# Performance work log

Hardware: AMD Instinct MI355X
Metric: run time of the kernel (lower is better)

Reference implementation:

```python
import jax, jax.numpy as jnp
import numpy as np

DIM = 1024
NUM_HEADS = 16
HEAD_DIM = DIM // NUM_HEADS
B, S = 2, 2048


def setup_inputs() -> dict:
    key = jax.random.key(0)
    ks = jax.random.split(key, 7)
    x = jax.random.normal(ks[0], (B, S, DIM), dtype=jnp.float32)
    cos = jax.random.uniform(ks[1], (S, HEAD_DIM // 2), dtype=jnp.float32)
    sin = jax.random.uniform(ks[2], (S, HEAD_DIM // 2), dtype=jnp.float32)
    scale = 1.0 / np.sqrt(DIM)
    Wq = jax.random.normal(ks[3], (DIM, DIM), dtype=jnp.float32) * scale
    Wk = jax.random.normal(ks[4], (DIM, DIM), dtype=jnp.float32) * scale
    Wv = jax.random.normal(ks[5], (DIM, DIM), dtype=jnp.float32) * scale
    Wo = jax.random.normal(ks[6], (DIM, DIM), dtype=jnp.float32) * scale
    return {"x": x, "cos": cos, "sin": sin, "Wq": Wq, "Wk": Wk, "Wv": Wv, "Wo": Wo}


def _apply_rope(t, c, s):
    # t: [B, S, H, hd]; c, s: [1, S, 1, hd] (already doubled)
    half = t.shape[-1] // 2
    t1, t2 = t[..., :half], t[..., half:]
    rot = jnp.concatenate([-t2, t1], axis=-1)
    return t * c + rot * s


def reference(x, cos, sin, Wq, Wk, Wv, Wo):
    Bs, Ss, D = x.shape
    H, hd = NUM_HEADS, HEAD_DIM
    q = (x @ Wq).reshape(Bs, Ss, H, hd)
    k = (x @ Wk).reshape(Bs, Ss, H, hd)
    v = (x @ Wv).reshape(Bs, Ss, H, hd)
    # repeat(1,1,1,2) in torch tiles cos as [cos, cos] along last dim
    c = jnp.concatenate([cos, cos], axis=-1)[None, :, None, :]
    s = jnp.concatenate([sin, sin], axis=-1)[None, :, None, :]
    q = _apply_rope(q, c, s)
    k = _apply_rope(k, c, s)
    # SDPA, non-causal, scale 1/sqrt(hd)
    scores = jnp.einsum("bqhd,bkhd->bhqk", q, k) / jnp.sqrt(jnp.float32(hd))
    attn = jax.nn.softmax(scores, axis=-1)
    out = jnp.einsum("bhqk,bkhd->bqhd", attn, v).reshape(Bs, Ss, D)
    return out @ Wo
```

## Files before the change

### kernel.cpp

```cpp
#include <hip/hip_runtime.h>

#define B_  2
#define S_  2048
#define D_  1024
#define H_  16
#define HD_ 64
#define M_  (B_*S_)

typedef __bf16 bf16x8 __attribute__((ext_vector_type(8)));
typedef float  f32x4  __attribute__((ext_vector_type(4)));
typedef float  f32x16 __attribute__((ext_vector_type(16)));
typedef unsigned short ushort_t;

static __device__ __forceinline__ ushort_t f2bf(float f) {
  __bf16 b = (__bf16)f;
  return __builtin_bit_cast(ushort_t, b);
}
static __device__ __forceinline__ float bf2f(ushort_t u) {
  return (float)__builtin_bit_cast(__bf16, u);
}

typedef __attribute__((address_space(1))) const unsigned u32g;
typedef __attribute__((address_space(3))) unsigned u32l;
static __device__ __forceinline__ void gll16(const ushort_t* g, __bf16* l) {
  __builtin_amdgcn_global_load_lds((u32g*)g, (u32l*)l, 16, 0, 0);
}

__global__ __launch_bounds__(256) void convert_x(const float* __restrict__ x,
                                                 ushort_t* __restrict__ xb) {
  size_t e = ((size_t)blockIdx.x * 256 + threadIdx.x) * 8;
  float4 a = *(const float4*)(x + e);
  float4 b = *(const float4*)(x + e + 4);
  uint4 pk;
  pk.x = (unsigned)f2bf(a.x) | ((unsigned)f2bf(a.y) << 16);
  pk.y = (unsigned)f2bf(a.z) | ((unsigned)f2bf(a.w) << 16);
  pk.z = (unsigned)f2bf(b.x) | ((unsigned)f2bf(b.y) << 16);
  pk.w = (unsigned)f2bf(b.z) | ((unsigned)f2bf(b.w) << 16);
  *(uint4*)(xb + e) = pk;
}

__global__ __launch_bounds__(256) void transpose_w(const float* __restrict__ Wq,
                                                   const float* __restrict__ Wk,
                                                   const float* __restrict__ Wv,
                                                   const float* __restrict__ Wo,
                                                   ushort_t* __restrict__ Wqkvt,
                                                   ushort_t* __restrict__ Wot) {
  __shared__ __bf16 T[64][72];
  const int z = blockIdx.z;
  const float* W = (z == 0) ? Wq : (z == 1) ? Wk : (z == 2) ? Wv : Wo;
  ushort_t* Wt = (z < 3) ? (Wqkvt + (size_t)z * 1048576) : Wot;
  const int k0 = blockIdx.y * 64, n0 = blockIdx.x * 64;
  const int t = threadIdx.x, r = t >> 2, c16 = (t & 3) * 16;
#pragma unroll
  for (int i = 0; i < 4; i++) {
    float4 v = *(const float4*)(W + (size_t)(k0 + r) * D_ + n0 + c16 + i * 4);
    T[r][c16 + i*4 + 0] = (__bf16)v.x;
    T[r][c16 + i*4 + 1] = (__bf16)v.y;
    T[r][c16 + i*4 + 2] = (__bf16)v.z;
    T[r][c16 + i*4 + 3] = (__bf16)v.w;
  }
  __syncthreads();
  ushort_t vals[16];
#pragma unroll
  for (int i = 0; i < 16; i++) vals[i] = __builtin_bit_cast(ushort_t, T[c16 + i][r]);
  ushort_t* dst = Wt + (size_t)(n0 + r) * D_ + k0 + c16;
  *(uint4*)dst       = *(const uint4*)&vals[0];
  *(uint4*)(dst + 8) = *(const uint4*)&vals[8];
}

__global__ __launch_bounds__(256) void transpose_v(const ushort_t* __restrict__ Vb,
                                                   ushort_t* __restrict__ Vtg) {
  __shared__ __bf16 T[64][72];
  const int bh = blockIdx.y, kt = blockIdx.x;
  const int t = threadIdx.x, r = t >> 2, c16 = (t & 3) * 16;
  const ushort_t* src = Vb + ((size_t)bh * S_ + kt*64 + r) * 64 + c16;
  *(uint4*)&T[r][c16]     = *(const uint4*)src;
  *(uint4*)&T[r][c16 + 8] = *(const uint4*)(src + 8);
  __syncthreads();
  ushort_t vals[16];
#pragma unroll
  for (int i = 0; i < 16; i++) {
    int c = c16 + i;
    int k = ((c & 1) << 5) | (c >> 1);
    vals[i] = __builtin_bit_cast(ushort_t, T[k][r]);
  }
  ushort_t* dst = Vtg + ((size_t)bh * 64 + r) * S_ + kt*64 + c16;
  *(uint4*)dst       = *(const uint4*)&vals[0];
  *(uint4*)(dst + 8) = *(const uint4*)&vals[8];
}

template<int OMODE, int BN>
__global__ __launch_bounds__(256) void gemm_bf16(const ushort_t* __restrict__ A,
                                                 const ushort_t* __restrict__ Bt,
                                                 void* __restrict__ Cp,
                                                 const float* __restrict__ cosb,
                                                 const float* __restrict__ sinb) {
  constexpr int NF = BN / 32;
  __shared__ __bf16 As[4096];
  __shared__ __bf16 Bs[BN * 32];
  const int t = threadIdx.x, w = t >> 6, lane = t & 63, l15 = lane & 15, g = lane >> 4;
  const int wr = w >> 1, wc = w & 1;
  const int row0 = blockIdx.y * 128, col0 = blockIdx.x * BN;
  const int lr = t >> 2, lc = (t & 3) * 8;
  f32x4 acc[4][NF] = {};

  for (int k0 = 0; k0 < D_; k0 += 32) {
    __syncthreads();
#pragma unroll
    for (int i = 0; i < 2; i++)
      gll16(A + (size_t)(row0 + i*64 + lr) * D_ + k0 + lc, &As[i*2048 + w*512]);
#pragma unroll
    for (int i = 0; i < BN/64; i++)
      gll16(Bt + (size_t)(col0 + i*64 + lr) * D_ + k0 + lc, &Bs[i*2048 + w*512]);
    __syncthreads();
    bf16x8 af[4], bfv[NF];
#pragma unroll
    for (int mt = 0; mt < 4; mt++)  af[mt]  = *(const bf16x8*)&As[(wr*64 + mt*16 + l15)*32 + g*8];
#pragma unroll
    for (int nt = 0; nt < NF; nt++) bfv[nt] = *(const bf16x8*)&Bs[(wc*(BN/2) + nt*16 + l15)*32 + g*8];
#pragma unroll
    for (int mt = 0; mt < 4; mt++)
#pragma unroll
      for (int nt = 0; nt < NF; nt++)
        acc[mt][nt] = __builtin_amdgcn_mfma_f32_16x16x32_bf16(af[mt], bfv[nt], acc[mt][nt], 0, 0, 0);
  }

  if (OMODE == 0) {
#pragma unroll
    for (int mt = 0; mt < 4; mt++)
#pragma unroll
      for (int nt = 0; nt < NF; nt++) {
        int col = col0 + wc*(BN/2) + nt*16 + l15;
#pragma unroll
        for (int reg = 0; reg < 4; reg++) {
          int r = row0 + wr*64 + mt*16 + g*4 + reg;
          ((float*)Cp)[(size_t)r * D_ + col] = acc[mt][nt][reg];
        }
      }
  } else {
    const int mat = col0 >> 10;
    const int nc0 = (col0 + wc*64) & 1023;
    const int h = nc0 >> 6;
    ushort_t* dst = (ushort_t*)Cp + (size_t)mat * 4194304;
    const float QS = 0.125f * 1.4426950408889634f;
#pragma unroll
    for (int mt = 0; mt < 4; mt++) {
#pragma unroll
      for (int reg = 0; reg < 4; reg++) {
        int r = row0 + wr*64 + mt*16 + g*4 + reg;
        int b = r >> 11, s = r & (S_ - 1);
        size_t base = (((size_t)(b*H_ + h) * S_ + s) << 6);
        if (mat < 2) {
#pragma unroll
          for (int nt = 0; nt < 2; nt++) {
            int d1 = nt*16 + l15;
            float c  = cosb[s*32 + d1];
            float sn = sinb[s*32 + d1];
            float v1 = acc[mt][nt][reg], v2 = acc[mt][nt+2][reg];
            float r1 = v1*c - v2*sn;
            float r2 = v2*c + v1*sn;
            if (mat == 0) { r1 *= QS; r2 *= QS; }
            dst[base + d1]      = f2bf(r1);
            dst[base + d1 + 32] = f2bf(r2);
          }
        } else {
#pragma unroll
          for (int nt = 0; nt < 4; nt++)
            dst[base + nt*16 + l15] = f2bf(acc[mt][nt][reg]);
        }
      }
    }
  }
}

__global__ __launch_bounds__(256) void attn32(const ushort_t* __restrict__ Q,
                                              const ushort_t* __restrict__ K,
                                              const ushort_t* __restrict__ Vtg,
                                              ushort_t* __restrict__ op0,
                                              ushort_t* __restrict__ op1,
                                              float* __restrict__ lw) {
  __shared__ __bf16 KsL[128 * 64];
  __shared__ __bf16 VtL[64 * 128];
  __shared__ __bf16 Ps[4][32][72];
  const int t = threadIdx.x, w = t >> 6, lane = t & 63;
  const int l31 = lane & 31, h2 = lane >> 5, sw = l31 & 7;
  const int bh = blockIdx.y, q0 = blockIdx.x * 128 + w * 32, z = blockIdx.z;

  const ushort_t* Qp = Q + ((size_t)bh * S_ + q0 + l31) * HD_;
  bf16x8 qf[4];
#pragma unroll
  for (int kc = 0; kc < 4; kc++) qf[kc] = *(const bf16x8*)(Qp + kc*16 + h2*8);

  f32x16 o0 = {}, o1 = {};
  float lp[16];
#pragma unroll
  for (int i = 0; i < 16; i++) lp[i] = 0.f;

  const ushort_t* Kb = K   + ((size_t)bh * S_ + z * 1024) * HD_;
  const ushort_t* Vg = Vtg + (size_t)bh * HD_ * S_ + z * 1024;

  const int krl = lane >> 3;
  const int kco = ((lane & 7) ^ krl) * 8;
  const int vrl = lane >> 4;

  for (int kt = 0; kt < 8; kt++) {
    __syncthreads();
#pragma unroll
    for (int p = 0; p < 4; p++) {
      int bk = w*8 + p*32;
      gll16(Kb + (size_t)(kt*128 + bk + krl) * HD_ + kco, &KsL[(bk)*64]);
    }
#pragma unroll
    for (int p = 0; p < 4; p++) {
      int bd = w*4 + p*16;
      int d  = bd + vrl;
      int cd = (lane & 8) | ((lane & 7) ^ (d & 7));
      gll16(Vg + (size_t)d * S_ + kt*128 + cd*8, &VtL[(bd)*128]);
    }
    __syncthreads();

#pragma unroll
    for (int ph = 0; ph < 2; ph++) {
      f32x16 s0 = {}, s1 = {};
#pragma unroll
      for (int kc = 0; kc < 4; kc++) {
        int c = kc*2 + h2;
        int cs = (c ^ sw) * 8;
        bf16x8 b0 = *(const bf16x8*)&KsL[(ph*64 + l31)*64      + cs];
        bf16x8 b1 = *(const bf16x8*)&KsL[(ph*64 + 32 + l31)*64 + cs];
        s0 = __builtin_amdgcn_mfma_f32_32x32x16_bf16(qf[kc], b0, s0, 0, 0, 0);
        s1 = __builtin_amdgcn_mfma_f32_32x32x16_bf16(qf[kc], b1, s1, 0, 0, 0);
      }

#pragma unroll
      for (int i = 0; i < 16; i++) {
        float p0 = __builtin_amdgcn_exp2f(s0[i]);
        float p1 = __builtin_amdgcn_exp2f(s1[i]);
        lp[i] += p0 + p1;
        int row = (i & 3) + 8*(i >> 2) + 4*h2;
        unsigned pk = (unsigned)f2bf(p0) | ((unsigned)f2bf(p1) << 16);
        *(unsigned*)&Ps[w][row][2*l31] = pk;
      }

#pragma unroll
      for (int kc = 0; kc < 4; kc++) {
        int c = kc*2 + h2;
        int cs = (ph*8 | (c ^ sw)) * 8;
        bf16x8 pf = *(const bf16x8*)&Ps[w][l31][kc*16 + h2*8];
        bf16x8 v0 = *(const bf16x8*)&VtL[(l31)*128      + cs];
        bf16x8 v1 = *(const bf16x8*)&VtL[(32 + l31)*128 + cs];
        o0 = __builtin_amdgcn_mfma_f32_32x32x16_bf16(pf, v0, o0, 0, 0, 0);
        o1 = __builtin_amdgcn_mfma_f32_32x32x16_bf16(pf, v1, o1, 0, 0, 0);
      }
    }
  }

#pragma unroll
  for (int i = 0; i < 16; i++) {
#pragma unroll
    for (int mk = 1; mk < 32; mk <<= 1) lp[i] += __shfl_xor(lp[i], mk, 64);
  }

  ushort_t* op = (z == 0) ? op0 : op1;
  float* lwp = lw + (size_t)(z*32 + bh) * S_;
#pragma unroll
  for (int i = 0; i < 16; i++) {
    int row = q0 + (i & 3) + 8*(i >> 2) + 4*h2;
    size_t base = ((size_t)bh * S_ + row) * 64;
    op[base + l31]      = f2bf(o0[i]);
    op[base + 32 + l31] = f2bf(o1[i]);
    if (l31 == 0) lwp[row] = lp[i];
  }
}

__global__ __launch_bounds__(256) void combine(const ushort_t* __restrict__ op0,
                                               const ushort_t* __restrict__ op1,
                                               const float* __restrict__ lw,
                                               ushort_t* __restrict__ att) {
  int tid = blockIdx.x * 256 + threadIdx.x;
  int d8 = (tid & 7) * 8;
  int s  = (tid >> 3) & (S_ - 1);
  int bh = tid >> 14;
  size_t pb = ((size_t)bh * S_ + s) * 64 + d8;
  uint4 a = *(const uint4*)(op0 + pb);
  uint4 b = *(const uint4*)(op1 + pb);
  float inv = 1.f / (lw[(size_t)bh * S_ + s] + lw[(size_t)(32 + bh) * S_ + s]);
  const ushort_t* as = (const ushort_t*)&a;
  const ushort_t* bs = (const ushort_t*)&b;
  ushort_t outv[8];
#pragma unroll
  for (int i = 0; i < 8; i++)
    outv[i] = f2bf((bf2f(as[i]) + bf2f(bs[i])) * inv);
  int bidx = bh >> 4, h = bh & 15;
  *(uint4*)(att + ((size_t)(bidx * S_ + s)) * D_ + h*64 + d8) = *(const uint4*)outv;
}

extern "C" void kernel_launch(void* const* d_in, const int* in_sizes, int n_in,
                              void* d_out, int out_size, void* d_ws, size_t ws_size,
                              hipStream_t stream) {
  (void)in_sizes; (void)n_in; (void)out_size; (void)ws_size;
  const float* x    = (const float*)d_in[0];
  const float* cosb = (const float*)d_in[1];
  const float* sinb = (const float*)d_in[2];
  const float* Wq   = (const float*)d_in[3];
  const float* Wk   = (const float*)d_in[4];
  const float* Wv   = (const float*)d_in[5];
  const float* Wo   = (const float*)d_in[6];
  float* out = (float*)d_out;

  ushort_t* w     = (ushort_t*)d_ws;
  ushort_t* xb    = w;
  ushort_t* Wqkvt = w + 4194304;
  ushort_t* Wot   = w + 7340032;
  ushort_t* Qb    = w + 8388608;
  ushort_t* Kb    = w + 12582912;
  ushort_t* Vb    = w + 16777216;
  ushort_t* Vtg   = w + 20971520;
  ushort_t* att   = w + 25165824;
  float*    lw    = (float*)Wqkvt;

  convert_x<<<2048, 256, 0, stream>>>(x, xb);
  transpose_w<<<dim3(16, 16, 4), 256, 0, stream>>>(Wq, Wk, Wv, Wo, Wqkvt, Wot);

  gemm_bf16<1,128><<<dim3(24, 32), 256, 0, stream>>>(xb, Wqkvt, Qb, cosb, sinb);

  transpose_v<<<dim3(32, 32), 256, 0, stream>>>(Vb, Vtg);

  attn32<<<dim3(16, 32, 2), 256, 0, stream>>>(Qb, Kb, Vtg, xb, Vb, lw);

  combine<<<2048, 256, 0, stream>>>(xb, Vb, lw, att);

  gemm_bf16<0,64><<<dim3(16, 32), 256, 0, stream>>>(att, Wot, out, nullptr, nullptr);
}
```

Baseline: 214.5 us.

## Swap GEMM operand roles with LDS-staged coalesced epilogue and double-buffer attention K/V

```diff
diff --git a/kernel.cpp b/kernel.cpp
--- a/kernel.cpp
+++ b/kernel.cpp
@@ -89,39 +89,41 @@
   *(uint4*)(dst + 8) = *(const uint4*)&vals[8];
 }
 
-template<int OMODE, int BN>
-__global__ __launch_bounds__(256) void gemm_bf16(const ushort_t* __restrict__ A,
-                                                 const ushort_t* __restrict__ Bt,
+template<int OMODE, int BS>
+__global__ __launch_bounds__(256) void gemm_bf16(const ushort_t* __restrict__ Wt,
+                                                 const ushort_t* __restrict__ X,
                                                  void* __restrict__ Cp,
                                                  const float* __restrict__ cosb,
                                                  const float* __restrict__ sinb) {
-  constexpr int NF = BN / 32;
-  __shared__ __bf16 As[4096];
-  __shared__ __bf16 Bs[BN * 32];
+  constexpr int NT = BS / 32;
+  constexpr int SM = (OMODE == 1) ? 16384 : 6144;
+  __shared__ __bf16 SMEM[SM];
+  __bf16* As = SMEM;
+  __bf16* Bs = SMEM + 4096;
   const int t = threadIdx.x, w = t >> 6, lane = t & 63, l15 = lane & 15, g = lane >> 4;
   const int wr = w >> 1, wc = w & 1;
-  const int row0 = blockIdx.y * 128, col0 = blockIdx.x * BN;
-  const int lr = t >> 2, lc = (t & 3) * 8;
-  f32x4 acc[4][NF] = {};
+  const int f0 = blockIdx.y * 128, s0 = blockIdx.x * BS;
+  const int al = lane >> 2, ac = (lane & 3) * 8;
+  f32x4 acc[4][NT] = {};
 
   for (int k0 = 0; k0 < D_; k0 += 32) {
     __syncthreads();
 #pragma unroll
     for (int i = 0; i < 2; i++)
-      gll16(A + (size_t)(row0 + i*64 + lr) * D_ + k0 + lc, &As[i*2048 + w*512]);
-#pragma unroll
-    for (int i = 0; i < BN/64; i++)
-      gll16(Bt + (size_t)(col0 + i*64 + lr) * D_ + k0 + lc, &Bs[i*2048 + w*512]);
+      gll16(Wt + (size_t)(f0 + i*64 + w*16 + al) * D_ + k0 + ac, &As[i*2048 + w*512]);
+#pragma unroll
+    for (int i = 0; i < BS/64; i++)
+      gll16(X + (size_t)(s0 + i*64 + w*16 + al) * D_ + k0 + ac, &Bs[i*2048 + w*512]);
     __syncthreads();
-    bf16x8 af[4], bfv[NF];
+    bf16x8 af[4], bfv[NT];
 #pragma unroll
     for (int mt = 0; mt < 4; mt++)  af[mt]  = *(const bf16x8*)&As[(wr*64 + mt*16 + l15)*32 + g*8];
 #pragma unroll
-    for (int nt = 0; nt < NF; nt++) bfv[nt] = *(const bf16x8*)&Bs[(wc*(BN/2) + nt*16 + l15)*32 + g*8];
+    for (int nt = 0; nt < NT; nt++) bfv[nt] = *(const bf16x8*)&Bs[(wc*(BS/2) + nt*16 + l15)*32 + g*8];
 #pragma unroll
     for (int mt = 0; mt < 4; mt++)
 #pragma unroll
-      for (int nt = 0; nt < NF; nt++)
+      for (int nt = 0; nt < NT; nt++)
         acc[mt][nt] = __builtin_amdgcn_mfma_f32_16x16x32_bf16(af[mt], bfv[nt], acc[mt][nt], 0, 0, 0);
   }
 
@@ -129,46 +131,61 @@
 #pragma unroll
     for (int mt = 0; mt < 4; mt++)
 #pragma unroll
-      for (int nt = 0; nt < NF; nt++) {
-        int col = col0 + wc*(BN/2) + nt*16 + l15;
-#pragma unroll
-        for (int reg = 0; reg < 4; reg++) {
-          int r = row0 + wr*64 + mt*16 + g*4 + reg;
-          ((float*)Cp)[(size_t)r * D_ + col] = acc[mt][nt][reg];
-        }
+      for (int nt = 0; nt < NT; nt++) {
+        int s = s0 + wc*(BS/2) + nt*16 + l15;
+        int f = f0 + wr*64 + mt*16 + g*4;
+        *(float4*)&((float*)Cp)[(size_t)s * D_ + f] = *(float4*)&acc[mt][nt];
       }
   } else {
-    const int mat = col0 >> 10;
-    const int nc0 = (col0 + wc*64) & 1023;
-    const int h = nc0 >> 6;
+    const int hid = blockIdx.y*2 + wr;
+    const int mat = hid >> 4, h = hid & 15;
+    const int s0w = s0 + wc*64;
     ushort_t* dst = (ushort_t*)Cp + (size_t)mat * 4194304;
     const float QS = 0.125f * 1.4426950408889634f;
-#pragma unroll
-    for (int mt = 0; mt < 4; mt++) {
-#pragma unroll
-      for (int reg = 0; reg < 4; reg++) {
-        int r = row0 + wr*64 + mt*16 + g*4 + reg;
-        int b = r >> 11, s = r & (S_ - 1);
-        size_t base = (((size_t)(b*H_ + h) * S_ + s) << 6);
-        if (mat < 2) {
-#pragma unroll
-          for (int nt = 0; nt < 2; nt++) {
-            int d1 = nt*16 + l15;
-            float c  = cosb[s*32 + d1];
-            float sn = sinb[s*32 + d1];
-            float v1 = acc[mt][nt][reg], v2 = acc[mt][nt+2][reg];
-            float r1 = v1*c - v2*sn;
-            float r2 = v2*c + v1*sn;
+    if (mat < 2) {
+#pragma unroll
+      for (int mt = 0; mt < 2; mt++)
+#pragma unroll
+        for (int nt = 0; nt < 4; nt++) {
+          int s  = s0w + nt*16 + l15;
+          int sq = s & (S_ - 1);
+          float4 c4 = *(const float4*)&cosb[sq*32 + mt*16 + g*4];
+          float4 s4 = *(const float4*)&sinb[sq*32 + mt*16 + g*4];
+          const float* cf = (const float*)&c4;
+          const float* sf = (const float*)&s4;
+#pragma unroll
+          for (int r = 0; r < 4; r++) {
+            float v1 = acc[mt][nt][r], v2 = acc[mt+2][nt][r];
+            float r1 = v1*cf[r] - v2*sf[r];
+            float r2 = v2*cf[r] + v1*sf[r];
             if (mat == 0) { r1 *= QS; r2 *= QS; }
-            dst[base + d1]      = f2bf(r1);
-            dst[base + d1 + 32] = f2bf(r2);
+            acc[mt][nt][r] = r1; acc[mt+2][nt][r] = r2;
           }
-        } else {
-#pragma unroll
-          for (int nt = 0; nt < 4; nt++)
-            dst[base + nt*16 + l15] = f2bf(acc[mt][nt][reg]);
         }
+    }
+    __syncthreads();
+    __bf16* Tw = SMEM + w*4096;
+#pragma unroll
+    for (int mt = 0; mt < 4; mt++)
+#pragma unroll
+      for (int nt = 0; nt < 4; nt++) {
+        int s_loc = nt*16 + l15;
+        int d0 = mt*16 + g*4;
+        int ch = (d0 >> 3) ^ (s_loc & 7);
+        ushort_t pk[4];
+#pragma unroll
+        for (int r = 0; r < 4; r++) pk[r] = f2bf(acc[mt][nt][r]);
+        *(ushort4*)&Tw[s_loc*64 + ch*8 + (d0 & 7)] = *(const ushort4*)pk;
       }
+#pragma unroll
+    for (int j = 0; j < 8; j++) {
+      int s_loc = j*8 + (lane >> 3);
+      int ci = lane & 7;
+      int ch = ci ^ (s_loc & 7);
+      uint4 v = *(const uint4*)&Tw[s_loc*64 + ch*8];
+      int s = s0w + s_loc;
+      int b = s >> 11, srow = s & (S_ - 1);
+      *(uint4*)&dst[(((size_t)(b*H_ + h) * S_ + srow) << 6) + ci*8] = v;
     }
   }
 }
@@ -179,8 +196,8 @@
                                               ushort_t* __restrict__ op0,
                                               ushort_t* __restrict__ op1,
                                               float* __restrict__ lw) {
-  __shared__ __bf16 KsL[128 * 64];
-  __shared__ __bf16 VtL[64 * 128];
+  __shared__ __bf16 KsL[2][64 * 64];
+  __shared__ __bf16 VtL[2][64 * 64];
   __shared__ __bf16 Ps[4][32][72];
   const int t = threadIdx.x, w = t >> 6, lane = t & 63;
   const int l31 = lane & 31, h2 = lane >> 5, sw = l31 & 7;
@@ -198,62 +215,69 @@
 
   const ushort_t* Kb = K   + ((size_t)bh * S_ + z * 1024) * HD_;
   const ushort_t* Vg = Vtg + (size_t)bh * HD_ * S_ + z * 1024;
-
   const int krl = lane >> 3;
   const int kco = ((lane & 7) ^ krl) * 8;
-  const int vrl = lane >> 4;
-
-  for (int kt = 0; kt < 8; kt++) {
-    __syncthreads();
-#pragma unroll
-    for (int p = 0; p < 4; p++) {
-      int bk = w*8 + p*32;
-      gll16(Kb + (size_t)(kt*128 + bk + krl) * HD_ + kco, &KsL[(bk)*64]);
-    }
-#pragma unroll
-    for (int p = 0; p < 4; p++) {
-      int bd = w*4 + p*16;
-      int d  = bd + vrl;
-      int cd = (lane & 8) | ((lane & 7) ^ (d & 7));
-      gll16(Vg + (size_t)d * S_ + kt*128 + cd*8, &VtL[(bd)*128]);
-    }
-    __syncthreads();
-
-#pragma unroll
-    for (int ph = 0; ph < 2; ph++) {
-      f32x16 s0 = {}, s1 = {};
-#pragma unroll
-      for (int kc = 0; kc < 4; kc++) {
-        int c = kc*2 + h2;
-        int cs = (c ^ sw) * 8;
-        bf16x8 b0 = *(const bf16x8*)&KsL[(ph*64 + l31)*64      + cs];
-        bf16x8 b1 = *(const bf16x8*)&KsL[(ph*64 + 32 + l31)*64 + cs];
-        s0 = __builtin_amdgcn_mfma_f32_32x32x16_bf16(qf[kc], b0, s0, 0, 0, 0);
-        s1 = __builtin_amdgcn_mfma_f32_32x32x16_bf16(qf[kc], b1, s1, 0, 0, 0);
-      }
-
-#pragma unroll
-      for (int i = 0; i < 16; i++) {
-        float p0 = __builtin_amdgcn_exp2f(s0[i]);
-        float p1 = __builtin_amdgcn_exp2f(s1[i]);
-        lp[i] += p0 + p1;
-        int row = (i & 3) + 8*(i >> 2) + 4*h2;
-        unsigned pk = (unsigned)f2bf(p0) | ((unsigned)f2bf(p1) << 16);
-        *(unsigned*)&Ps[w][row][2*l31] = pk;
-      }
-
-#pragma unroll
-      for (int kc = 0; kc < 4; kc++) {
-        int c = kc*2 + h2;
-        int cs = (ph*8 | (c ^ sw)) * 8;
-        bf16x8 pf = *(const bf16x8*)&Ps[w][l31][kc*16 + h2*8];
-        bf16x8 v0 = *(const bf16x8*)&VtL[(l31)*128      + cs];
-        bf16x8 v1 = *(const bf16x8*)&VtL[(32 + l31)*128 + cs];
-        o0 = __builtin_amdgcn_mfma_f32_32x32x16_bf16(pf, v0, o0, 0, 0, 0);
-        o1 = __builtin_amdgcn_mfma_f32_32x32x16_bf16(pf, v1, o1, 0, 0, 0);
-      }
-    }
-  }
+
+  asm volatile("s_waitcnt vmcnt(0)" ::: "memory");
+
+#define STAGE(KT, CB)                                                        \
+  {                                                                          \
+    _Pragma("unroll")                                                        \
+    for (int p = 0; p < 2; p++) {                                            \
+      int bk = w*8 + p*32;                                                   \
+      gll16(Kb + (size_t)((KT)*64 + bk + krl) * HD_ + kco, &KsL[CB][bk*64]); \
+    }                                                                        \
+    _Pragma("unroll")                                                        \
+    for (int p = 0; p < 2; p++) {                                            \
+      int bd = w*8 + p*32;                                                   \
+      gll16(Vg + (size_t)(bd + krl) * S_ + (KT)*64 + kco, &VtL[CB][bd*64]);  \
+    }                                                                        \
+  }
+
+  STAGE(0, 0);
+  for (int kt = 0; kt < 16; kt++) {
+    const int cur = kt & 1;
+    if (kt < 15) {
+      STAGE(kt + 1, cur ^ 1);
+      asm volatile("s_waitcnt vmcnt(4)" ::: "memory");
+    } else {
+      asm volatile("s_waitcnt vmcnt(0)" ::: "memory");
+    }
+    asm volatile("s_barrier" ::: "memory");
+
+    f32x16 s0 = {}, s1 = {};
+#pragma unroll
+    for (int kc = 0; kc < 4; kc++) {
+      int cs = ((kc*2 + h2) ^ sw) * 8;
+      bf16x8 b0 = *(const bf16x8*)&KsL[cur][l31*64 + cs];
+      bf16x8 b1 = *(const bf16x8*)&KsL[cur][(32 + l31)*64 + cs];
+      s0 = __builtin_amdgcn_mfma_f32_32x32x16_bf16(qf[kc], b0, s0, 0, 0, 0);
+      s1 = __builtin_amdgcn_mfma_f32_32x32x16_bf16(qf[kc], b1, s1, 0, 0, 0);
+    }
+
+#pragma unroll
+    for (int i = 0; i < 16; i++) {
+      float p0 = __builtin_amdgcn_exp2f(s0[i]);
+      float p1 = __builtin_amdgcn_exp2f(s1[i]);
+      lp[i] += p0 + p1;
+      int row = (i & 3) + 8*(i >> 2) + 4*h2;
+      unsigned pk = (unsigned)f2bf(p0) | ((unsigned)f2bf(p1) << 16);
+      *(unsigned*)&Ps[w][row][2*l31] = pk;
+    }
+
+#pragma unroll
+    for (int kc = 0; kc < 4; kc++) {
+      int cs = ((kc*2 + h2) ^ sw) * 8;
+      bf16x8 pf = *(const bf16x8*)&Ps[w][l31][kc*16 + h2*8];
+      bf16x8 v0 = *(const bf16x8*)&VtL[cur][l31*64 + cs];
+      bf16x8 v1 = *(const bf16x8*)&VtL[cur][(32 + l31)*64 + cs];
+      o0 = __builtin_amdgcn_mfma_f32_32x32x16_bf16(pf, v0, o0, 0, 0, 0);
+      o1 = __builtin_amdgcn_mfma_f32_32x32x16_bf16(pf, v1, o1, 0, 0, 0);
+    }
+
+    asm volatile("s_barrier" ::: "memory");
+  }
+#undef STAGE
 
 #pragma unroll
   for (int i = 0; i < 16; i++) {
@@ -322,7 +346,7 @@
   convert_x<<<2048, 256, 0, stream>>>(x, xb);
   transpose_w<<<dim3(16, 16, 4), 256, 0, stream>>>(Wq, Wk, Wv, Wo, Wqkvt, Wot);
 
-  gemm_bf16<1,128><<<dim3(24, 32), 256, 0, stream>>>(xb, Wqkvt, Qb, cosb, sinb);
+  gemm_bf16<1,128><<<dim3(32, 24), 256, 0, stream>>>(Wqkvt, xb, Qb, cosb, sinb);
 
   transpose_v<<<dim3(32, 32), 256, 0, stream>>>(Vb, Vtg);
 
@@ -330,5 +354,5 @@
 
   combine<<<2048, 256, 0, stream>>>(xb, Vb, lw, att);
 
-  gemm_bf16<0,64><<<dim3(16, 32), 256, 0, stream>>>(att, Wot, out, nullptr, nullptr);
-}
+  gemm_bf16<0,64><<<dim3(64, 8), 256, 0, stream>>>(Wot, att, out, nullptr, nullptr);
+}
```

Result: slower. 229.0 us (+6.7%).
